# Optimization experiments

Hardware: AMD Instinct MI355X
Metric: run time of the kernel (lower is better)

## Reference

```python
import jax, jax.numpy as jnp
import numpy as np

B, T, D_IN, H, D_OUT = 64, 2048, 128, 256, 128


def setup_inputs() -> dict:
    key = jax.random.key(0)
    ks = jax.random.split(key, 12)
    s_ih0 = 1.0 / np.sqrt(H)
    return {
        "x": jax.random.normal(ks[0], (B, T, D_IN), dtype=jnp.float32),
        "W_ih0": jax.random.normal(ks[1], (H, D_IN), dtype=jnp.float32) * s_ih0,
        "W_hh0": jax.random.normal(ks[2], (H, H), dtype=jnp.float32) * s_ih0,
        "b_ih0": jax.random.normal(ks[3], (H,), dtype=jnp.float32) * s_ih0,
        "b_hh0": jax.random.normal(ks[4], (H,), dtype=jnp.float32) * s_ih0,
        "W_ih1": jax.random.normal(ks[5], (H, H), dtype=jnp.float32) * s_ih0,
        "W_hh1": jax.random.normal(ks[6], (H, H), dtype=jnp.float32) * s_ih0,
        "b_ih1": jax.random.normal(ks[7], (H,), dtype=jnp.float32) * s_ih0,
        "b_hh1": jax.random.normal(ks[8], (H,), dtype=jnp.float32) * s_ih0,
        "fc_w": jax.random.normal(ks[9], (D_OUT, H), dtype=jnp.float32) * s_ih0,
        "fc_b": jax.random.normal(ks[10], (D_OUT,), dtype=jnp.float32) * s_ih0,
    }


def _rnn_layer(inp_tbd, W_ih, W_hh, b_ih, b_hh):
    # inp_tbd: [T, B, D]; PyTorch RNN: h_t = tanh(x_t W_ih^T + b_ih + h_{t-1} W_hh^T + b_hh)
    # Precompute the input projection for all timesteps in one GEMM.
    pre = jnp.einsum("tbd,hd->tbh", inp_tbd, W_ih) + b_ih + b_hh  # [T, B, H]
    h0 = jnp.zeros((inp_tbd.shape[1], W_hh.shape[0]), dtype=inp_tbd.dtype)

    def step(h, p):
        h_new = jnp.tanh(p + h @ W_hh.T)
        return h_new, h_new

    _, hs = jax.lax.scan(step, h0, pre)  # hs: [T, B, H]
    return hs


def reference(x, W_ih0, W_hh0, b_ih0, b_hh0, W_ih1, W_hh1, b_ih1, b_hh1, fc_w, fc_b):
    xt = jnp.transpose(x, (1, 0, 2))  # [T, B, D_IN] (batch_first -> time-major)
    h1 = _rnn_layer(xt, W_ih0, W_hh0, b_ih0, b_hh0)   # layer 0
    h2 = _rnn_layer(h1, W_ih1, W_hh1, b_ih1, b_hh1)   # layer 1
    last = h2[-1]  # [B, H] == out[:, -1, :]
    return last @ fc_w.T + fc_b  # [B, D_OUT]
```

## Files before the change

### kernel.cpp

```cpp
#include <hip/hip_runtime.h>

typedef _Float16 f16;
typedef _Float16 f16x4 __attribute__((ext_vector_type(4)));
typedef _Float16 f16x8 __attribute__((ext_vector_type(8)));
typedef __fp16   fp16x2 __attribute__((ext_vector_type(2)));
typedef float    f32x4 __attribute__((ext_vector_type(4)));

#define MFMA_F16(A,B,C) __builtin_amdgcn_mfma_f32_16x16x32_f16((A),(B),(C),0,0,0)

#define C2F 2.885390081777927f

__device__ __forceinline__ f16x4 pk4(float a, float b, float c, float d) {
  union { fp16x2 p[2]; f16x4 v; } u;
  u.p[0] = __builtin_amdgcn_cvt_pkrtz(a, b);
  u.p[1] = __builtin_amdgcn_cvt_pkrtz(c, d);
  return u.v;
}

__device__ __forceinline__ int pslot(int s) {
  return s ^ (((s >> 3) & 1) << 2) ^ (((s >> 4) & 1) << 1);
}


__global__ void prep_kernel(const float* __restrict__ Wih0, const float* __restrict__ Whh0,
                            const float* __restrict__ Wih1, const float* __restrict__ Whh1,
                            const float* __restrict__ bih0, const float* __restrict__ bhh0,
                            const float* __restrict__ bih1, const float* __restrict__ bhh1,
                            f16* __restrict__ wdst, float* __restrict__ b0C, float* __restrict__ b1C)
{
  if (blockIdx.x == 224) {
    const int i = threadIdx.x;
    b0C[i] = (bih0[i] + bhh0[i]) * C2F;
    b1C[i] = (bih1[i] + bhh1[i]) * C2F;
    return;
  }
  const int i4 = (blockIdx.x * 256 + threadIdx.x) * 4;
  const float* src; int off;
  if (i4 < 32768)       { src = Wih0; off = i4; }
  else if (i4 < 98304)  { src = Whh0; off = i4 - 32768; }
  else if (i4 < 163840) { src = Wih1; off = i4 - 98304; }
  else                  { src = Whh1; off = i4 - 163840; }
  const float4 v = *(const float4*)(src + off);
  *(f16x4*)(wdst + i4) = pk4(v.x, v.y, v.z, v.w);
}

template<int KK, int MODE>
__global__ __launch_bounds__(256, 2)
void gemm_proj(const void* Asrc, const f16* __restrict__ W,
               const float* __restrict__ biasC, f16* outp)
{
  constexpr int NKB = KK / 32;
  __shared__ f16 sB[4 * NKB * 512];

  const int tid = threadIdx.x, lane = tid & 63, wv = tid >> 6;
  const int l15 = lane & 15, l4 = lane >> 4;
  const int bid = blockIdx.x;

  if constexpr (MODE == 0) {
    const float* x = (const float*)Asrc + ((size_t)(bid >> 5) * 2048 + (size_t)(bid & 31) * 64) * 128;
    const int rp = tid >> 3, kg = tid & 7;
#pragma unroll
    for (int rr = 0; rr < 2; ++rr) {
      const int row = rp * 2 + rr;
      const float* xr = x + (size_t)row * 128 + kg * 16;
#pragma unroll
      for (int c4 = 0; c4 < 4; ++c4) {
        const float4 v = *(const float4*)(xr + c4 * 4);
        const int k = kg * 16 + c4 * 4;
        const int rt = row >> 4, kb = k >> 5;
        const int slot = (row & 15) + 16 * ((k >> 3) & 3);
        *(f16x4*)&sB[rt * (NKB * 512) + kb * 512 + slot * 8 + (k & 7)] = pk4(v.x, v.y, v.z, v.w);
      }
    }
  } else {
    const f16* hp = (const f16*)Asrc + (size_t)bid * 16384;
#pragma unroll
    for (int it = 0; it < 8; ++it) {
      const int o = tid * 8 + it * 2048;
      const f16x8 v = *(const f16x8*)(hp + o);
      const int cp = o >> 8;
      const int b0 = (o >> 2) & 63;
      const int k0 = cp * 4;
      const int kb = k0 >> 5;
      const int jo = k0 & 7;
      const int qq = (k0 >> 3) & 3;
      f16x4 lo; lo.x = v[0]; lo.y = v[1]; lo.z = v[2]; lo.w = v[3];
      f16x4 hi; hi.x = v[4]; hi.y = v[5]; hi.z = v[6]; hi.w = v[7];
      const int s0 = ((b0 & 15) + 16 * qq), rt0 = b0 >> 4;
      const int s1 = (((b0 + 1) & 15) + 16 * qq), rt1 = (b0 + 1) >> 4;
      *(f16x4*)&sB[rt0 * (NKB * 512) + kb * 512 + s0 * 8 + jo] = lo;
      *(f16x4*)&sB[rt1 * (NKB * 512) + kb * 512 + s1 * 8 + jo] = hi;
    }
  }
  __syncthreads();

  f16x8 wa[4][NKB];
#pragma unroll
  for (int ct = 0; ct < 4; ++ct) {
    const int oc = wv * 64 + ct * 16 + l15;
#pragma unroll
    for (int kb = 0; kb < NKB; ++kb)
      wa[ct][kb] = *(const f16x8*)(W + (size_t)oc * KK + kb * 32 + l4 * 8);
  }
  float bC[4][4];
#pragma unroll
  for (int ct = 0; ct < 4; ++ct)
#pragma unroll
    for (int r = 0; r < 4; ++r)
      bC[ct][r] = biasC[wv * 64 + ct * 16 + l4 * 4 + r];

  f32x4 acc[4][4];
#pragma unroll
  for (int ct = 0; ct < 4; ++ct)
#pragma unroll
    for (int rt = 0; rt < 4; ++rt)
      acc[ct][rt] = f32x4{0.f, 0.f, 0.f, 0.f};

#pragma unroll
  for (int kb = 0; kb < NKB; ++kb)
#pragma unroll
    for (int rt = 0; rt < 4; ++rt) {
      const f16x8 hb = *(const f16x8*)&sB[rt * (NKB * 512) + kb * 512 + lane * 8];
#pragma unroll
      for (int ct = 0; ct < 4; ++ct)
        acc[ct][rt] = MFMA_F16(wa[ct][kb], hb, acc[ct][rt]);
    }

#pragma unroll
  for (int rt = 0; rt < 4; ++rt) {
    const int rown = rt * 16 + l15;
    size_t base;
    if constexpr (MODE == 0) base = ((size_t)(bid & 31) * 64 + rown) * 16384 + (size_t)(bid >> 5) * 4;
    else                     base = (size_t)bid * 16384 + (size_t)rown * 4;
#pragma unroll
    for (int ct = 0; ct < 4; ++ct) {
      const int cp = wv * 16 + ct * 4 + l4;
      const float v0 = fmaf(acc[ct][rt][0], C2F, bC[ct][0]);
      const float v1 = fmaf(acc[ct][rt][1], C2F, bC[ct][1]);
      const float v2 = fmaf(acc[ct][rt][2], C2F, bC[ct][2]);
      const float v3 = fmaf(acc[ct][rt][3], C2F, bC[ct][3]);
      *(f16x4*)(outp + base + (size_t)cp * 256) = pk4(v0, v1, v2, v3);
    }
  }
}

template<int LAYER>
__global__ __launch_bounds__(512, 2)
void rnn_rec(const f16* pre,
             const f16* __restrict__ Whh,
             f16* hout,
             float* __restrict__ hlast)
{
  __shared__ f16 sH[8192];
  const int tid = threadIdx.x, lane = tid & 63, wv = tid >> 6;
  const int l15 = lane & 15, l4 = lane >> 4;
  const int g16 = blockIdx.x * 16;

  for (int i = tid; i < 2048; i += 512) ((unsigned int*)sH)[i] = 0u;

  f16x8 wa[2][8];
#pragma unroll
  for (int ct = 0; ct < 2; ++ct) {
    const int oc = wv * 32 + ct * 16 + l15;
#pragma unroll
    for (int kb = 0; kb < 8; ++kb)
      wa[ct][kb] = *(const f16x8*)(Whh + (size_t)oc * 256 + kb * 32 + l4 * 8);
  }

  int woff[2];
#pragma unroll
  for (int ct = 0; ct < 2; ++ct) {
    const int q = ct * 2 + (l4 >> 1);
    woff[ct] = wv * 512 + pslot(l15 + 16 * q) * 8 + (l4 & 1) * 4;
  }
  const int roff = pslot(lane) * 8;

  const int laneP = (wv * 8 + l4) * 256 + (g16 + l15) * 4;

  f16x4 pA[2], pB[2];
#pragma unroll
  for (int ct = 0; ct < 2; ++ct) {
    pA[ct] = *(const f16x4*)(pre + laneP + ct * 1024);
    pB[ct] = *(const f16x4*)(pre + 16384 + laneP + ct * 1024);
  }
  __syncthreads();

  auto step = [&](int t, int rdo, int wro, f16x4 (&pc)[2], bool last) {
    f32x4 acc[2];
#pragma unroll
    for (int i = 0; i < 2; ++i) acc[i] = f32x4{0.f, 0.f, 0.f, 0.f};
#pragma unroll
    for (int kb = 0; kb < 8; ++kb) {
      const f16x8 hb = *(const f16x8*)&sH[rdo + kb * 512 + roff];
#pragma unroll
      for (int ct = 0; ct < 2; ++ct)
        acc[ct] = MFMA_F16(wa[ct][kb], hb, acc[ct]);
    }
    float z2[2][4];
#pragma unroll
    for (int ct = 0; ct < 2; ++ct)
#pragma unroll
      for (int r = 0; r < 4; ++r)
        z2[ct][r] = fmaf(acc[ct][r], C2F, (float)pc[ct][r]);
    if (t + 2 < 2048) {
#pragma unroll
      for (int ct = 0; ct < 2; ++ct)
        pc[ct] = *(const f16x4*)(pre + (size_t)(t + 2) * 16384 + laneP + ct * 1024);
    }
#pragma unroll
    for (int ct = 0; ct < 2; ++ct) {
      float h[4];
#pragma unroll
      for (int r = 0; r < 4; ++r) {
        const float e = __builtin_amdgcn_exp2f(z2[ct][r]);
        h[r] = fmaf(__builtin_amdgcn_rcpf(e + 1.0f), -2.0f, 1.0f);
      }
      const f16x4 pk = pk4(h[0], h[1], h[2], h[3]);
      *(f16x4*)&sH[wro + woff[ct]] = pk;
      if constexpr (LAYER == 0) {
        *(f16x4*)(hout + (size_t)t * 16384 + laneP + ct * 1024) = pk;
      } else {
        if (last) {
#pragma unroll
          for (int r = 0; r < 4; ++r)
            hlast[(g16 + l15) * 256 + wv * 32 + ct * 16 + l4 * 4 + r] = h[r];
        }
      }
    }
    asm volatile("s_waitcnt lgkmcnt(0)" ::: "memory");
    __builtin_amdgcn_sched_barrier(0);
    __builtin_amdgcn_s_barrier();
    __builtin_amdgcn_sched_barrier(0);
  };

#pragma unroll 1
  for (int t = 0; t < 2048; t += 2) {
    step(t,     0,    4096, pA, false);
    step(t + 1, 4096, 0,    pB, t + 1 == 2047);
  }
}

__global__ void fc_kernel(const float* __restrict__ h, const float* __restrict__ W,
                          const float* __restrict__ bvec, float* __restrict__ out)
{
  const int idx = blockIdx.x * 256 + threadIdx.x;
  const int bb = idx >> 7, o = idx & 127;
  const float4* hp = (const float4*)(h + bb * 256);
  const float4* wp = (const float4*)(W + o * 256);
  float acc = 0.f;
#pragma unroll
  for (int i = 0; i < 64; ++i) {
    const float4 a = hp[i], c = wp[i];
    acc += a.x * c.x + a.y * c.y + a.z * c.z + a.w * c.w;
  }
  out[idx] = acc + bvec[o];
}

extern "C" void kernel_launch(void* const* d_in, const int* in_sizes, int n_in,
                              void* d_out, int out_size, void* d_ws, size_t ws_size,
                              hipStream_t stream)
{
  const float* x    = (const float*)d_in[0];
  const float* Wih0 = (const float*)d_in[1];
  const float* Whh0 = (const float*)d_in[2];
  const float* bih0 = (const float*)d_in[3];
  const float* bhh0 = (const float*)d_in[4];
  const float* Wih1 = (const float*)d_in[5];
  const float* Whh1 = (const float*)d_in[6];
  const float* bih1 = (const float*)d_in[7];
  const float* bhh1 = (const float*)d_in[8];
  const float* fcw  = (const float*)d_in[9];
  const float* fcb  = (const float*)d_in[10];
  float* out = (float*)d_out;

  char* ws = (char*)d_ws;
  f16*   Wih0h  = (f16*)(ws);
  f16*   Whh0h  = (f16*)(ws + 65536);
  f16*   Wih1h  = (f16*)(ws + 196608);
  f16*   Whh1h  = (f16*)(ws + 327680);
  float* b0C    = (float*)(ws + 458752);
  float* b1C    = (float*)(ws + 459776);
  float* h2last = (float*)(ws + 460800);
  f16*   buf    = (f16*)(ws + 526336);

  prep_kernel<<<225, 256, 0, stream>>>(Wih0, Whh0, Wih1, Whh1, bih0, bhh0, bih1, bhh1,
                                       Wih0h, b0C, b1C);
  gemm_proj<128, 0><<<2048, 256, 0, stream>>>(x,   Wih0h, b0C, buf);
  rnn_rec<0><<<4, 512, 0, stream>>>(buf, Whh0h, buf, nullptr);
  gemm_proj<256, 1><<<2048, 256, 0, stream>>>(buf, Wih1h, b1C, buf);
  rnn_rec<1><<<4, 512, 0, stream>>>(buf, Whh1h, nullptr, h2last);
  fc_kernel<<<32, 256, 0, stream>>>(h2last, fcw, fcb, out);
}
```

Before: 2.468 ms.

## Fuse both RNN layers into one skewed recurrent kernel, dropping layer-1 projection GEMM

Replaces the two sequential recurrence kernels and the layer-1 input projection GEMM with a single kernel that runs layer 1 one timestep behind layer 0. Each tick computes layer 0's recurrence and layer 1's input and recurrent products from shared-memory hidden states, followed by a final tail step. This removes one full serial 2048-step chain and the global round-trip of layer-0 outputs. In exchange, each step carries three times the MFMA work and holds three weight matrices in registers.

```diff
diff --git a/kernel.cpp b/kernel.cpp
--- a/kernel.cpp
+++ b/kernel.cpp
@@ -44,25 +44,24 @@
   *(f16x4*)(wdst + i4) = pk4(v.x, v.y, v.z, v.w);
 }
 
-template<int KK, int MODE>
 __global__ __launch_bounds__(256, 2)
-void gemm_proj(const void* Asrc, const f16* __restrict__ W,
-               const float* __restrict__ biasC, f16* outp)
-{
-  constexpr int NKB = KK / 32;
+void gemm_proj0(const float* __restrict__ x, const f16* __restrict__ W,
+                const float* __restrict__ biasC, f16* __restrict__ outp)
+{
+  constexpr int NKB = 4;
   __shared__ f16 sB[4 * NKB * 512];
 
   const int tid = threadIdx.x, lane = tid & 63, wv = tid >> 6;
   const int l15 = lane & 15, l4 = lane >> 4;
   const int bid = blockIdx.x;
 
-  if constexpr (MODE == 0) {
-    const float* x = (const float*)Asrc + ((size_t)(bid >> 5) * 2048 + (size_t)(bid & 31) * 64) * 128;
+  {
+    const float* xp = x + ((size_t)(bid >> 5) * 2048 + (size_t)(bid & 31) * 64) * 128;
     const int rp = tid >> 3, kg = tid & 7;
 #pragma unroll
     for (int rr = 0; rr < 2; ++rr) {
       const int row = rp * 2 + rr;
-      const float* xr = x + (size_t)row * 128 + kg * 16;
+      const float* xr = xp + (size_t)row * 128 + kg * 16;
 #pragma unroll
       for (int c4 = 0; c4 < 4; ++c4) {
         const float4 v = *(const float4*)(xr + c4 * 4);
@@ -72,25 +71,6 @@
         *(f16x4*)&sB[rt * (NKB * 512) + kb * 512 + slot * 8 + (k & 7)] = pk4(v.x, v.y, v.z, v.w);
       }
     }
-  } else {
-    const f16* hp = (const f16*)Asrc + (size_t)bid * 16384;
-#pragma unroll
-    for (int it = 0; it < 8; ++it) {
-      const int o = tid * 8 + it * 2048;
-      const f16x8 v = *(const f16x8*)(hp + o);
-      const int cp = o >> 8;
-      const int b0 = (o >> 2) & 63;
-      const int k0 = cp * 4;
-      const int kb = k0 >> 5;
-      const int jo = k0 & 7;
-      const int qq = (k0 >> 3) & 3;
-      f16x4 lo; lo.x = v[0]; lo.y = v[1]; lo.z = v[2]; lo.w = v[3];
-      f16x4 hi; hi.x = v[4]; hi.y = v[5]; hi.z = v[6]; hi.w = v[7];
-      const int s0 = ((b0 & 15) + 16 * qq), rt0 = b0 >> 4;
-      const int s1 = (((b0 + 1) & 15) + 16 * qq), rt1 = (b0 + 1) >> 4;
-      *(f16x4*)&sB[rt0 * (NKB * 512) + kb * 512 + s0 * 8 + jo] = lo;
-      *(f16x4*)&sB[rt1 * (NKB * 512) + kb * 512 + s1 * 8 + jo] = hi;
-    }
   }
   __syncthreads();
 
@@ -100,7 +80,7 @@
     const int oc = wv * 64 + ct * 16 + l15;
 #pragma unroll
     for (int kb = 0; kb < NKB; ++kb)
-      wa[ct][kb] = *(const f16x8*)(W + (size_t)oc * KK + kb * 32 + l4 * 8);
+      wa[ct][kb] = *(const f16x8*)(W + (size_t)oc * 128 + kb * 32 + l4 * 8);
   }
   float bC[4][4];
 #pragma unroll
@@ -129,9 +109,7 @@
 #pragma unroll
   for (int rt = 0; rt < 4; ++rt) {
     const int rown = rt * 16 + l15;
-    size_t base;
-    if constexpr (MODE == 0) base = ((size_t)(bid & 31) * 64 + rown) * 16384 + (size_t)(bid >> 5) * 4;
-    else                     base = (size_t)bid * 16384 + (size_t)rown * 4;
+    const size_t base = ((size_t)(bid & 31) * 64 + rown) * 16384 + (size_t)(bid >> 5) * 4;
 #pragma unroll
     for (int ct = 0; ct < 4; ++ct) {
       const int cp = wv * 16 + ct * 4 + l4;
@@ -144,28 +122,39 @@
   }
 }
 
-template<int LAYER>
 __global__ __launch_bounds__(512, 2)
-void rnn_rec(const f16* pre,
-             const f16* __restrict__ Whh,
-             f16* hout,
-             float* __restrict__ hlast)
-{
-  __shared__ f16 sH[8192];
+void fused_rnn(const f16* __restrict__ pre,
+               const f16* __restrict__ Whh0,
+               const f16* __restrict__ Wih1,
+               const f16* __restrict__ Whh1,
+               const float* __restrict__ b1C,
+               float* __restrict__ hlast)
+{
+  __shared__ f16 sH[16384];
   const int tid = threadIdx.x, lane = tid & 63, wv = tid >> 6;
   const int l15 = lane & 15, l4 = lane >> 4;
   const int g16 = blockIdx.x * 16;
 
   for (int i = tid; i < 2048; i += 512) ((unsigned int*)sH)[i] = 0u;
-
-  f16x8 wa[2][8];
+  for (int i = tid; i < 4096; i += 512) ((unsigned int*)sH)[4096 + i] = 0u;
+
+  f16x8 wa0[2][8], wi1[2][8], wh1[2][8];
 #pragma unroll
   for (int ct = 0; ct < 2; ++ct) {
-    const int oc = wv * 32 + ct * 16 + l15;
-#pragma unroll
-    for (int kb = 0; kb < 8; ++kb)
-      wa[ct][kb] = *(const f16x8*)(Whh + (size_t)oc * 256 + kb * 32 + l4 * 8);
-  }
+    const size_t oc = (size_t)(wv * 32 + ct * 16 + l15) * 256;
+#pragma unroll
+    for (int kb = 0; kb < 8; ++kb) {
+      wa0[ct][kb] = *(const f16x8*)(Whh0 + oc + kb * 32 + l4 * 8);
+      wi1[ct][kb] = *(const f16x8*)(Wih1 + oc + kb * 32 + l4 * 8);
+      wh1[ct][kb] = *(const f16x8*)(Whh1 + oc + kb * 32 + l4 * 8);
+    }
+  }
+  float b1r[2][4];
+#pragma unroll
+  for (int ct = 0; ct < 2; ++ct)
+#pragma unroll
+    for (int r = 0; r < 4; ++r)
+      b1r[ct][r] = b1C[wv * 32 + ct * 16 + l4 * 4 + r];
 
   int woff[2];
 #pragma unroll
@@ -185,23 +174,30 @@
   }
   __syncthreads();
 
-  auto step = [&](int t, int rdo, int wro, f16x4 (&pc)[2], bool last) {
-    f32x4 acc[2];
-#pragma unroll
-    for (int i = 0; i < 2; ++i) acc[i] = f32x4{0.f, 0.f, 0.f, 0.f};
-#pragma unroll
-    for (int kb = 0; kb < 8; ++kb) {
-      const f16x8 hb = *(const f16x8*)&sH[rdo + kb * 512 + roff];
-#pragma unroll
-      for (int ct = 0; ct < 2; ++ct)
-        acc[ct] = MFMA_F16(wa[ct][kb], hb, acc[ct]);
-    }
-    float z2[2][4];
+  auto tick = [&](int t, int h0r, int h0w, int h1r, int h1w, f16x4 (&pc)[2]) {
+    f32x4 a0[2], a1[2];
+#pragma unroll
+    for (int i = 0; i < 2; ++i) { a0[i] = f32x4{0.f,0.f,0.f,0.f}; a1[i] = f32x4{0.f,0.f,0.f,0.f}; }
+#pragma unroll
+    for (int kb = 0; kb < 8; ++kb) {
+      const f16x8 hb = *(const f16x8*)&sH[h0r + kb * 512 + roff];
+      a0[0] = MFMA_F16(wa0[0][kb], hb, a0[0]);
+      a0[1] = MFMA_F16(wa0[1][kb], hb, a0[1]);
+      a1[0] = MFMA_F16(wi1[0][kb], hb, a1[0]);
+      a1[1] = MFMA_F16(wi1[1][kb], hb, a1[1]);
+    }
+#pragma unroll
+    for (int kb = 0; kb < 8; ++kb) {
+      const f16x8 hb = *(const f16x8*)&sH[h1r + kb * 512 + roff];
+      a1[0] = MFMA_F16(wh1[0][kb], hb, a1[0]);
+      a1[1] = MFMA_F16(wh1[1][kb], hb, a1[1]);
+    }
+    float z0[2][4];
 #pragma unroll
     for (int ct = 0; ct < 2; ++ct)
 #pragma unroll
       for (int r = 0; r < 4; ++r)
-        z2[ct][r] = fmaf(acc[ct][r], C2F, (float)pc[ct][r]);
+        z0[ct][r] = fmaf(a0[ct][r], C2F, (float)pc[ct][r]);
     if (t + 2 < 2048) {
 #pragma unroll
       for (int ct = 0; ct < 2; ++ct)
@@ -212,20 +208,20 @@
       float h[4];
 #pragma unroll
       for (int r = 0; r < 4; ++r) {
-        const float e = __builtin_amdgcn_exp2f(z2[ct][r]);
+        const float e = __builtin_amdgcn_exp2f(z0[ct][r]);
         h[r] = fmaf(__builtin_amdgcn_rcpf(e + 1.0f), -2.0f, 1.0f);
       }
-      const f16x4 pk = pk4(h[0], h[1], h[2], h[3]);
-      *(f16x4*)&sH[wro + woff[ct]] = pk;
-      if constexpr (LAYER == 0) {
-        *(f16x4*)(hout + (size_t)t * 16384 + laneP + ct * 1024) = pk;
-      } else {
-        if (last) {
-#pragma unroll
-          for (int r = 0; r < 4; ++r)
-            hlast[(g16 + l15) * 256 + wv * 32 + ct * 16 + l4 * 4 + r] = h[r];
-        }
+      *(f16x4*)&sH[h0w + woff[ct]] = pk4(h[0], h[1], h[2], h[3]);
+    }
+#pragma unroll
+    for (int ct = 0; ct < 2; ++ct) {
+      float h[4];
+#pragma unroll
+      for (int r = 0; r < 4; ++r) {
+        const float e = __builtin_amdgcn_exp2f(fmaf(a1[ct][r], C2F, b1r[ct][r]));
+        h[r] = fmaf(__builtin_amdgcn_rcpf(e + 1.0f), -2.0f, 1.0f);
       }
+      if (t > 0) *(f16x4*)&sH[h1w + woff[ct]] = pk4(h[0], h[1], h[2], h[3]);
     }
     asm volatile("s_waitcnt lgkmcnt(0)" ::: "memory");
     __builtin_amdgcn_sched_barrier(0);
@@ -235,8 +231,34 @@
 
 #pragma unroll 1
   for (int t = 0; t < 2048; t += 2) {
-    step(t,     0,    4096, pA, false);
-    step(t + 1, 4096, 0,    pB, t + 1 == 2047);
+    tick(t,     0,    4096, 8192,  12288, pA);
+    tick(t + 1, 4096, 0,    12288, 8192,  pB);
+  }
+
+  {
+    f32x4 a1[2];
+#pragma unroll
+    for (int i = 0; i < 2; ++i) a1[i] = f32x4{0.f,0.f,0.f,0.f};
+#pragma unroll
+    for (int kb = 0; kb < 8; ++kb) {
+      const f16x8 hb = *(const f16x8*)&sH[0 + kb * 512 + roff];
+      a1[0] = MFMA_F16(wi1[0][kb], hb, a1[0]);
+      a1[1] = MFMA_F16(wi1[1][kb], hb, a1[1]);
+    }
+#pragma unroll
+    for (int kb = 0; kb < 8; ++kb) {
+      const f16x8 hb = *(const f16x8*)&sH[8192 + kb * 512 + roff];
+      a1[0] = MFMA_F16(wh1[0][kb], hb, a1[0]);
+      a1[1] = MFMA_F16(wh1[1][kb], hb, a1[1]);
+    }
+#pragma unroll
+    for (int ct = 0; ct < 2; ++ct)
+#pragma unroll
+      for (int r = 0; r < 4; ++r) {
+        const float e = __builtin_amdgcn_exp2f(fmaf(a1[ct][r], C2F, b1r[ct][r]));
+        const float h = fmaf(__builtin_amdgcn_rcpf(e + 1.0f), -2.0f, 1.0f);
+        hlast[(g16 + l15) * 256 + wv * 32 + ct * 16 + l4 * 4 + r] = h;
+      }
   }
 }
 
@@ -285,9 +307,7 @@
 
   prep_kernel<<<225, 256, 0, stream>>>(Wih0, Whh0, Wih1, Whh1, bih0, bhh0, bih1, bhh1,
                                        Wih0h, b0C, b1C);
-  gemm_proj<128, 0><<<2048, 256, 0, stream>>>(x,   Wih0h, b0C, buf);
-  rnn_rec<0><<<4, 512, 0, stream>>>(buf, Whh0h, buf, nullptr);
-  gemm_proj<256, 1><<<2048, 256, 0, stream>>>(buf, Wih1h, b1C, buf);
-  rnn_rec<1><<<4, 512, 0, stream>>>(buf, Whh1h, nullptr, h2last);
+  gemm_proj0<<<2048, 256, 0, stream>>>(x, Wih0h, b0C, buf);
+  fused_rnn<<<4, 512, 0, stream>>>(buf, Whh0h, Wih1h, Whh1h, b1C, h2last);
   fc_kernel<<<32, 256, 0, stream>>>(h2last, fcw, fcb, out);
 }
```

Result: slower. 3.440 ms (+39.4%).
